# Kernel optimization log

Hardware: AMD Instinct MI355X
Metric: run time of the kernel (lower is better)

The kernel has to match this reference:

```python
import jax, jax.numpy as jnp
import numpy as np

B, K, C, H, W = 16, 32, 256, 80, 80
NH, HD = 8, 32          # num_heads, head_dim (C = NH*HD)
S = 4                   # fixed roi_align sampling grid per 1x1 output bin
EPS = 1e-5


def _bn(x, g, b, m, v):
    # inference-mode BatchNorm2d, NCHW
    s = g / jnp.sqrt(v + EPS)
    return x * s[None, :, None, None] + (b - m * s)[None, :, None, None]


def _bilinear(feat, ys, xs):
    # feat [B,C,H,W]; ys,xs [B,K,S,S] -> [B,K,S,S,C], torchvision roi_align semantics
    Hh, Ww = feat.shape[2], feat.shape[3]
    valid = (ys >= -1.0) & (ys <= Hh) & (xs >= -1.0) & (xs <= Ww)
    y = jnp.clip(ys, 0.0, Hh - 1.0)
    x = jnp.clip(xs, 0.0, Ww - 1.0)
    y0 = jnp.floor(y); x0 = jnp.floor(x)
    y0i = y0.astype(jnp.int32); x0i = x0.astype(jnp.int32)
    y1i = jnp.minimum(y0i + 1, Hh - 1); x1i = jnp.minimum(x0i + 1, Ww - 1)
    ly = y - y0; lx = x - x0; hy = 1.0 - ly; hx = 1.0 - lx
    bidx = jnp.arange(feat.shape[0])[:, None, None, None]
    g = lambda yi, xi: feat[bidx, :, yi, xi]  # -> [B,K,S,S,C]
    val = ((hy * hx)[..., None] * g(y0i, x0i) + (hy * lx)[..., None] * g(y0i, x1i)
           + (ly * hx)[..., None] * g(y1i, x0i) + (ly * lx)[..., None] * g(y1i, x1i))
    return val * valid[..., None].astype(val.dtype)


def _roi_align_1x1(feat, boxes):
    # boxes [B,K,4] normalized xyxy; spatial_scale = 1.0 in the source
    Hh, Ww = feat.shape[2], feat.shape[3]
    sc = jnp.asarray([Ww - 1, Hh - 1, Ww - 1, Hh - 1], feat.dtype)
    ab = boxes * sc
    x1, y1, x2, y2 = ab[..., 0], ab[..., 1], ab[..., 2], ab[..., 3]
    rw = jnp.maximum(x2 - x1, 1.0)
    rh = jnp.maximum(y2 - y1, 1.0)
    grid = (jnp.arange(S, dtype=feat.dtype) + 0.5) / S
    ys = y1[..., None] + grid * rh[..., None]   # [B,K,S]
    xs = x1[..., None] + grid * rw[..., None]
    ys2, xs2 = jnp.broadcast_arrays(ys[..., :, None], xs[..., None, :])  # [B,K,S,S]
    vals = _bilinear(feat, ys2, xs2)            # [B,K,S,S,C]
    return vals.mean(axis=(2, 3)).reshape(feat.shape[0] * boxes.shape[1], -1)


def _gat(nodes, wq, bq, wk, bkp, wv, bv, scale, wo, bo, ln_g, ln_b):
    Bk = nodes.shape[0]
    q = (nodes @ wq.T + bq).reshape(Bk, NH, HD)
    k = (nodes @ wk.T + bkp).reshape(Bk, NH, HD)
    v = (nodes @ wv.T + bv).reshape(Bk, NH, HD)
    scores = jnp.einsum('ihd,jhd->ijh', q, k) * scale
    attn = jax.nn.softmax(scores, axis=1)       # softmax over keys j
    msg = jnp.einsum('ijh,jhd->ihd', attn, v).reshape(Bk, NH * HD)
    y = nodes + msg @ wo.T + bo
    mu = y.mean(-1, keepdims=True)
    var = ((y - mu) ** 2).mean(-1, keepdims=True)
    return (y - mu) / jnp.sqrt(var + EPS) * ln_g + ln_b


def _forward(x, boxes, conv_w, conv_b, bn1_g, bn1_b, bn1_m, bn1_v,
             wq, bq, wk, bkp, wv, bv, scale, wo, bo, ln_g, ln_b,
             rec_w, rec_b, bn2_g, bn2_b, bn2_m, bn2_v):
    feat = jax.lax.conv_general_dilated(
        x, conv_w, (1, 1), 'SAME',
        dimension_numbers=('NCHW', 'OIHW', 'NCHW')) + conv_b[None, :, None, None]
    feat = _bn(feat, bn1_g, bn1_b, bn1_m, bn1_v)
    feat = feat * jax.nn.sigmoid(feat)          # SiLU
    nodes = _roi_align_1x1(feat, boxes)         # [B*K, C]
    enh = _gat(nodes, wq, bq, wk, bkp, wv, bv, scale, wo, bo, ln_g, ln_b)
    f = enh.reshape(B, K, C)
    wts = jax.nn.softmax(f.mean(-1), axis=1)    # [B,K]
    weighted = jnp.einsum('bkc,bk->bc', f, wts)
    # out map is spatially constant -> 1x1 conv + BN collapse to per-sample affine
    y = weighted @ rec_w[:, :, 0, 0].T + rec_b
    s = bn2_g / jnp.sqrt(bn2_v + EPS)
    y = y * s + (bn2_b - bn2_m * s)
    return x + y[:, :, None, None]


def setup_inputs() -> dict:
    key = jax.random.key(0)
    ks = jax.random.split(key, 10)
    x = jax.random.normal(ks[0], (B, C, H, W), jnp.float32)
    bx = jax.random.uniform(ks[1], (B, K, 4), jnp.float32)
    bx = bx.at[:, :, 2:].add(bx[:, :, :2])      # xy2 += xy1
    boxes = jnp.clip(bx, 0.0, 1.0)
    w = lambda k, shp: jax.random.normal(k, shp, jnp.float32) * 0.02
    return {
        'x': x, 'boxes': boxes,
        'conv_w': w(ks[2], (C, C, 3, 3)), 'conv_b': jnp.zeros((C,), jnp.float32),
        'bn1_g': jnp.ones((C,), jnp.float32), 'bn1_b': jnp.zeros((C,), jnp.float32),
        'bn1_m': jnp.zeros((C,), jnp.float32), 'bn1_v': jnp.ones((C,), jnp.float32),
        'wq': w(ks[3], (C, C)), 'bq': jnp.zeros((C,), jnp.float32),
        'wk': w(ks[4], (C, C)), 'bkp': jnp.zeros((C,), jnp.float32),
        'wv': w(ks[5], (C, C)), 'bv': jnp.zeros((C,), jnp.float32),
        'scale': jnp.asarray(1.0 / np.sqrt(HD), jnp.float32),
        'wo': w(ks[6], (C, C)), 'bo': jnp.zeros((C,), jnp.float32),
        'ln_g': jnp.ones((C,), jnp.float32), 'ln_b': jnp.zeros((C,), jnp.float32),
        'rec_w': w(ks[7], (C, C, 1, 1)), 'rec_b': jnp.zeros((C,), jnp.float32),
        'bn2_g': jnp.ones((C,), jnp.float32), 'bn2_b': jnp.zeros((C,), jnp.float32),
        'bn2_m': jnp.zeros((C,), jnp.float32), 'bn2_v': jnp.ones((C,), jnp.float32),
    }


def reference(x, boxes, conv_w, conv_b, bn1_g, bn1_b, bn1_m, bn1_v,
              wq, bq, wk, bkp, wv, bv, scale, wo, bo, ln_g, ln_b,
              rec_w, rec_b, bn2_g, bn2_b, bn2_m, bn2_v):
    return _forward(x, boxes, conv_w, conv_b, bn1_g, bn1_b, bn1_m, bn1_v,
                    wq, bq, wk, bkp, wv, bv, scale, wo, bo, ln_g, ln_b,
                    rec_w, rec_b, bn2_g, bn2_b, bn2_m, bn2_v)
```

## Files before the change

### kernel.cpp

```cpp
#include <hip/hip_runtime.h>

#define EPSV 1e-5f

typedef __attribute__((ext_vector_type(8))) short short8v;
typedef __attribute__((ext_vector_type(4))) float f32x4;

static __device__ __forceinline__ unsigned short f2bf(float f) {
  unsigned int u = __float_as_uint(f);
  u += 0x7fff + ((u >> 16) & 1);
  return (unsigned short)(u >> 16);
}
static __device__ __forceinline__ float bf2f(unsigned short h) {
  return __uint_as_float(((unsigned int)h) << 16);
}

static __device__ __forceinline__ void glds16(const void* g, void* l) {
  __builtin_amdgcn_global_load_lds(
      (const __attribute__((address_space(1))) void*)g,
      (__attribute__((address_space(3))) void*)l, 16, 0, 0);
}

__global__ __launch_bounds__(256) void prep_fused_kernel(
    const float* __restrict__ x, unsigned short* __restrict__ xin,
    const float* __restrict__ cw, unsigned short* __restrict__ Wr,
    float* __restrict__ zpad,
    const float* __restrict__ wq, const float* __restrict__ wk,
    const float* __restrict__ wv, const float* __restrict__ wo,
    const float* __restrict__ rec, float* __restrict__ wT)
{
  __shared__ unsigned short t[80 * 257];
  const int bid = blockIdx.x;
  if (bid < 1280) {
    int b = bid / 80, y = bid - b * 80;
    const float* src = x + (size_t)b * 256 * 6400 + y * 80;
    for (int e = threadIdx.x; e < 256 * 20; e += 256) {
      int c = e / 20;
      int px4 = e - c * 20;
      f32x4 v = *(const f32x4*)&src[(size_t)c * 6400 + px4 * 4];
#pragma unroll
      for (int j = 0; j < 4; ++j)
        t[(px4 * 4 + j) * 257 + c] = f2bf(v[j]);
    }
    __syncthreads();
    unsigned short* dst = xin + (size_t)bid * 80 * 256;
    for (int e = threadIdx.x; e < 80 * 32; e += 256) {
      int px = e >> 5;
      int c8 = e & 31;
      short8v v;
#pragma unroll
      for (int j = 0; j < 8; ++j) v[j] = t[px * 257 + c8 * 8 + j];
      *(short8v*)&dst[px * 256 + c8 * 8] = v;
    }
  } else if (bid < 3584) {
    if (bid == 1280) zpad[threadIdx.x] = 0.f;
    int idx = (bid - 1280) * 256 + threadIdx.x;
    int cil = idx & 31;
    int rest = idx >> 5;
    int co = rest & 255;
    int tcc = rest >> 8;
    int cc = tcc & 7;
    int tt = tcc >> 3;
    int dy = tt / 3, dx = tt - dy * 3;
    int ci = cc * 32 + cil;
    Wr[idx] = f2bf(cw[((co * 256 + ci) * 3 + dy) * 3 + dx]);
  } else {
    int idx = (bid - 3584) * 256 + threadIdx.x;
    int m = idx >> 16;
    int e = idx & 65535;
    int ci = e >> 8, co = e & 255;
    const float* src = (m == 0) ? wq : (m == 1) ? wk : (m == 2) ? wv
                     : (m == 3) ? wo : rec;
    wT[idx] = src[co * 256 + ci];
  }
}

__global__ __launch_bounds__(256, 2) void roiconv_kernel(
    const unsigned short* __restrict__ xin,
    const float* __restrict__ boxes,
    const float* __restrict__ convb,
    const float* __restrict__ bn1g, const float* __restrict__ bn1b,
    const float* __restrict__ bn1m, const float* __restrict__ bn1v,
    const unsigned short* __restrict__ Wr,
    float* __restrict__ nodes)
{
  const int bid = blockIdx.x;
  const int n = (bid & 7) * 64 + (bid >> 3);
  const int b = n >> 5;
  const int tid = threadIdx.x;
  const int w = tid >> 6, lane = tid & 63;
  const int bq = lane >> 4, r16 = lane & 15;

  __shared__ __align__(16) char lds[61696];
  float* wcoef = (float*)(lds + 61440);

  const int px = tid >> 2;
  const float* bx = boxes + n * 4;
  float x1 = bx[0] * 79.f, y1 = bx[1] * 79.f, x2 = bx[2] * 79.f, y2 = bx[3] * 79.f;
  float rwd = fmaxf(x2 - x1, 1.f), rh = fmaxf(y2 - y1, 1.f);
  int s = px >> 2;
  int sy = s >> 2, sx = s & 3;
  float yy = y1 + (sy + 0.5f) * 0.25f * rh;
  float xx = x1 + (sx + 0.5f) * 0.25f * rwd;
  bool valid = (yy >= -1.f) && (yy <= 80.f) && (xx >= -1.f) && (xx <= 80.f);
  float yc = fminf(fmaxf(yy, 0.f), 79.f), xc = fminf(fmaxf(xx, 0.f), 79.f);
  float y0f = floorf(yc), x0f = floorf(xc);
  int y0i = (int)y0f, x0i = (int)x0f;
  int y1i = min(y0i + 1, 79), x1i = min(x0i + 1, 79);
  float ly = yc - y0f, lx = xc - x0f, hy = 1.f - ly, hx = 1.f - lx;
  int py = (px & 2) ? y1i : y0i;
  int pxx = (px & 1) ? x1i : x0i;
  if ((tid & 3) == 0)
    wcoef[px] = ((px & 2) ? ly : hy) * ((px & 1) ? lx : hx) *
                (valid ? 0.0625f : 0.f);

  const int chunk = (tid & 3) ^ ((px >> 1) & 3);
  unsigned ioff[9];
#pragma unroll
  for (int t = 0; t < 9; ++t) {
    int dy = t / 3, dx = t - dy * 3;
    int cy = py + dy - 1, cx = pxx + dx - 1;
    bool ok = ((unsigned)cy < 80u) && ((unsigned)cx < 80u);
    ioff[t] = ok ? (unsigned)((((b * 80 + cy) * 80 + cx) * 256 + chunk * 8) * 2)
                 : 52428800u;
  }
  unsigned woff[4];
#pragma unroll
  for (int i = 0; i < 4; ++i) {
    int s2 = tid + (i << 8);
    int wco = s2 >> 2;
    int wch = (s2 & 3) ^ ((wco >> 1) & 3);
    woff[i] = (unsigned)((wco * 32 + wch * 8) * 2);
  }
  const int laneoff = r16 * 64 + ((bq ^ ((r16 >> 1) & 3)) << 4);
  const char* xinb = (const char*)xin;
  const char* Wrb = (const char*)Wr;
  const int ldst_in = (w << 6) << 4;

  f32x4 acc[4][4];
#pragma unroll
  for (int i = 0; i < 4; ++i)
#pragma unroll
    for (int j = 0; j < 4; ++j)
      acc[i][j] = (f32x4){0.f, 0.f, 0.f, 0.f};

  glds16(xinb + ioff[0], lds + 0 + ldst_in);
#pragma unroll
  for (int i = 0; i < 4; ++i)
    glds16(Wrb + woff[i], lds + 12288 + (((i << 8) + (w << 6)) << 4));
  glds16(xinb + ioff[1], lds + 4096 + ldst_in);
#pragma unroll
  for (int i = 0; i < 4; ++i)
    glds16(Wrb + ((size_t)8 << 14) + woff[i],
           lds + 28672 + (((i << 8) + (w << 6)) << 4));

  for (int cc = 0; cc < 8; ++cc) {
#pragma unroll
    for (int t = 0; t < 9; ++t) {
      const int cb = t % 3;
      const char* inb = lds + cb * 4096;
      const char* wb  = lds + 12288 + cb * 16384;
      if (cc == 7 && t == 8)
        asm volatile("s_waitcnt vmcnt(0)" ::: "memory");
      else
        asm volatile("s_waitcnt vmcnt(5)" ::: "memory");
      __builtin_amdgcn_s_barrier();
      __builtin_amdgcn_sched_barrier(0);
      if (!(cc == 7 && t >= 7)) {
        const int nt = (t + 2 > 8) ? t - 7 : t + 2;
        const int nb = nt % 3;
        const int ncc = cc + (t >= 7 ? 1 : 0);
        char* innx = lds + nb * 4096;
        char* wbn  = lds + 12288 + nb * 16384;
        glds16(xinb + ioff[nt] + ncc * 64, innx + ldst_in);
        const char* wg = Wrb + ((size_t)(nt * 8 + ncc) << 14);
#pragma unroll
        for (int i = 0; i < 4; ++i)
          glds16(wg + woff[i], wbn + (((i << 8) + (w << 6)) << 4));
      }
      const char* pa = inb + laneoff;
      const char* pw = wb + w * 4096 + laneoff;
      short8v af0 = *(const short8v*)(pa);
      short8v af1 = *(const short8v*)(pa + 1024);
      short8v af2 = *(const short8v*)(pa + 2048);
      short8v af3 = *(const short8v*)(pa + 3072);
      short8v wf0 = *(const short8v*)(pw);
      short8v wf1 = *(const short8v*)(pw + 1024);
      short8v wf2 = *(const short8v*)(pw + 2048);
      short8v wf3 = *(const short8v*)(pw + 3072);
      __builtin_amdgcn_s_setprio(1);
      acc[0][0] = __builtin_amdgcn_mfma_f32_16x16x32_bf16(af0, wf0, acc[0][0], 0, 0, 0);
      acc[0][1] = __builtin_amdgcn_mfma_f32_16x16x32_bf16(af0, wf1, acc[0][1], 0, 0, 0);
      acc[0][2] = __builtin_amdgcn_mfma_f32_16x16x32_bf16(af0, wf2, acc[0][2], 0, 0, 0);
      acc[0][3] = __builtin_amdgcn_mfma_f32_16x16x32_bf16(af0, wf3, acc[0][3], 0, 0, 0);
      acc[1][0] = __builtin_amdgcn_mfma_f32_16x16x32_bf16(af1, wf0, acc[1][0], 0, 0, 0);
      acc[1][1] = __builtin_amdgcn_mfma_f32_16x16x32_bf16(af1, wf1, acc[1][1], 0, 0, 0);
      acc[1][2] = __builtin_amdgcn_mfma_f32_16x16x32_bf16(af1, wf2, acc[1][2], 0, 0, 0);
      acc[1][3] = __builtin_amdgcn_mfma_f32_16x16x32_bf16(af1, wf3, acc[1][3], 0, 0, 0);
      acc[2][0] = __builtin_amdgcn_mfma_f32_16x16x32_bf16(af2, wf0, acc[2][0], 0, 0, 0);
      acc[2][1] = __builtin_amdgcn_mfma_f32_16x16x32_bf16(af2, wf1, acc[2][1], 0, 0, 0);
      acc[2][2] = __builtin_amdgcn_mfma_f32_16x16x32_bf16(af2, wf2, acc[2][2], 0, 0, 0);
      acc[2][3] = __builtin_amdgcn_mfma_f32_16x16x32_bf16(af2, wf3, acc[2][3], 0, 0, 0);
      acc[3][0] = __builtin_amdgcn_mfma_f32_16x16x32_bf16(af3, wf0, acc[3][0], 0, 0, 0);
      acc[3][1] = __builtin_amdgcn_mfma_f32_16x16x32_bf16(af3, wf1, acc[3][1], 0, 0, 0);
      acc[3][2] = __builtin_amdgcn_mfma_f32_16x16x32_bf16(af3, wf2, acc[3][2], 0, 0, 0);
      acc[3][3] = __builtin_amdgcn_mfma_f32_16x16x32_bf16(af3, wf3, acc[3][3], 0, 0, 0);
      __builtin_amdgcn_s_setprio(0);
    }
  }
  asm volatile("s_waitcnt vmcnt(0)" ::: "memory");
  __syncthreads();

  unsigned short* ep = (unsigned short*)lds;
#pragma unroll
  for (int cf = 0; cf < 4; ++cf) {
    int co = w * 64 + cf * 16 + r16;
    float sc = bn1g[co] / sqrtf(bn1v[co] + EPSV);
    float sh = bn1b[co] - bn1m[co] * sc;
    float cb = convb[co];
#pragma unroll
    for (int mf = 0; mf < 4; ++mf) {
#pragma unroll
      for (int rg = 0; rg < 4; ++rg) {
        int pxo = mf * 16 + bq * 4 + rg;
        float v = (acc[mf][cf][rg] + cb) * sc + sh;
        v = v / (1.f + __expf(-v));
        ep[pxo * 264 + co] = f2bf(v);
      }
    }
  }
  __syncthreads();
  const int c = tid;
  float val = 0.f;
#pragma unroll
  for (int p = 0; p < 64; ++p)
    val += wcoef[p] * bf2f(ep[p * 264 + c]);
  nodes[n * 256 + c] = val;
}

__global__ __launch_bounds__(256) void qkv_kernel(
    const float* __restrict__ nodes, const float* __restrict__ wT,
    const float* __restrict__ bq, const float* __restrict__ bk,
    const float* __restrict__ bv,
    float* __restrict__ q, float* __restrict__ k, float* __restrict__ v)
{
  const int blk = blockIdx.x;
  const int co = threadIdx.x;
  __shared__ float nd[4][256];
  for (int i = threadIdx.x; i < 1024; i += 256)
    nd[i >> 8][i & 255] = nodes[blk * 1024 + i];
  __syncthreads();
  float aq[4] = {0, 0, 0, 0};
  float ak[4] = {0, 0, 0, 0};
  float av[4] = {0, 0, 0, 0};
  const float* wqT = wT;
  const float* wkT = wT + 65536;
  const float* wvT = wT + 131072;
  for (int ci = 0; ci < 256; ++ci) {
    float wq_ = wqT[ci * 256 + co];
    float wk_ = wkT[ci * 256 + co];
    float wv_ = wvT[ci * 256 + co];
#pragma unroll
    for (int r = 0; r < 4; ++r) {
      float nv = nd[r][ci];
      aq[r] += nv * wq_;
      ak[r] += nv * wk_;
      av[r] += nv * wv_;
    }
  }
  float bq_ = bq[co], bk_ = bk[co], bv_ = bv[co];
#pragma unroll
  for (int r = 0; r < 4; ++r) {
    int n = blk * 4 + r;
    q[n * 256 + co] = aq[r] + bq_;
    k[n * 256 + co] = ak[r] + bk_;
    v[n * 256 + co] = av[r] + bv_;
  }
}

__global__ __launch_bounds__(256) void attn_mh_kernel(
    const float* __restrict__ q, const float* __restrict__ k,
    const float* __restrict__ v, const float* __restrict__ scale_p,
    float* __restrict__ msgs)
{
  const int bid = blockIdx.x;
  const int h = bid & 7, qc = bid >> 3;
  const int q0 = qc * 16;
  const int tid = threadIdx.x;
  __shared__ __align__(16) float Kh[512 * 32];
  __shared__ __align__(16) float Vh[512 * 32];
  __shared__ unsigned short pb[16 * 512];

  for (int idx = tid; idx < 4096; idx += 256) {
    int j = idx >> 3, part = idx & 7;
    int chs = part ^ (j & 7);
    *(f32x4*)&Kh[j * 32 + chs * 4] =
        *(const f32x4*)&k[(size_t)j * 256 + h * 32 + part * 4];
    *(f32x4*)&Vh[j * 32 + chs * 4] =
        *(const f32x4*)&v[(size_t)j * 256 + h * 32 + part * 4];
  }
  const int qi = tid >> 4, l = tid & 15;
  f32x4 qr[8];
#pragma unroll
  for (int p = 0; p < 8; ++p)
    qr[p] = *(const f32x4*)&q[(size_t)(q0 + qi) * 256 + h * 32 + p * 4];
  const float scale = scale_p[0];
  __syncthreads();

  float pj[32];
  float mx = -1e30f;
#pragma unroll
  for (int jj = 0; jj < 32; ++jj) {
    int j = jj * 16 + l;
    const float* kr = &Kh[j * 32];
    int sw = j & 7;
    float s = 0.f;
#pragma unroll
    for (int p = 0; p < 8; ++p) {
      f32x4 kv = *(const f32x4*)&kr[(p ^ sw) * 4];
      s += kv.x * qr[p].x + kv.y * qr[p].y + kv.z * qr[p].z + kv.w * qr[p].w;
    }
    s *= scale;
    pj[jj] = s;
    mx = fmaxf(mx, s);
  }
#pragma unroll
  for (int o = 1; o < 16; o <<= 1) mx = fmaxf(mx, __shfl_xor(mx, o, 16));
  float sum = 0.f;
#pragma unroll
  for (int jj = 0; jj < 32; ++jj) {
    float e = __expf(pj[jj] - mx);
    pj[jj] = e;
    sum += e;
  }
#pragma unroll
  for (int o = 1; o < 16; o <<= 1) sum += __shfl_xor(sum, o, 16);
  float inv = 1.f / sum;
#pragma unroll
  for (int jj = 0; jj < 32; ++jj)
    pb[qi * 512 + jj * 16 + l] = f2bf(pj[jj] * inv);
  __syncthreads();

  float m0 = 0.f, m1 = 0.f;
  const unsigned short* pq = &pb[qi * 512];
  for (int j = 0; j < 512; ++j) {
    float p = bf2f(pq[j]);
    int chs = (l >> 1) ^ (j & 7);
    const float* vr = &Vh[j * 32 + chs * 4 + ((2 * l) & 3)];
    m0 += p * vr[0];
    m1 += p * vr[1];
  }
  float* mo = &msgs[(size_t)(q0 + qi) * 256 + h * 32 + 2 * l];
  mo[0] = m0;
  mo[1] = m1;
}

__global__ __launch_bounds__(256) void outln_kernel(
    const float* __restrict__ msgs, const float* __restrict__ nodes,
    const float* __restrict__ woT, const float* __restrict__ bo,
    const float* __restrict__ lng, const float* __restrict__ lnb,
    float* __restrict__ enh)
{
  const int blk = blockIdx.x;
  const int co = threadIdx.x;
  __shared__ float ms[8][256];
  __shared__ float red1[8][4], red2[8][4];
  for (int i = co; i < 2048; i += 256)
    ms[i >> 8][i & 255] = msgs[blk * 2048 + i];
  __syncthreads();
  float yv[8];
  float bo_ = bo[co];
#pragma unroll
  for (int r = 0; r < 8; ++r)
    yv[r] = nodes[(size_t)(blk * 8 + r) * 256 + co] + bo_;
  for (int ci = 0; ci < 256; ++ci) {
    float w = woT[ci * 256 + co];
#pragma unroll
    for (int r = 0; r < 8; ++r) yv[r] += ms[r][ci] * w;
  }
  const int wv = co >> 6, lane = co & 63;
#pragma unroll
  for (int r = 0; r < 8; ++r) {
    float s1 = yv[r], s2 = yv[r] * yv[r];
#pragma unroll
    for (int o = 1; o < 64; o <<= 1) {
      s1 += __shfl_xor(s1, o);
      s2 += __shfl_xor(s2, o);
    }
    if (lane == 0) { red1[r][wv] = s1; red2[r][wv] = s2; }
  }
  __syncthreads();
  float lg = lng[co], lb = lnb[co];
#pragma unroll
  for (int r = 0; r < 8; ++r) {
    float S1 = red1[r][0] + red1[r][1] + red1[r][2] + red1[r][3];
    float S2 = red2[r][0] + red2[r][1] + red2[r][2] + red2[r][3];
    float mu = S1 * (1.f / 256.f);
    float var = S2 * (1.f / 256.f) - mu * mu;
    enh[(size_t)(blk * 8 + r) * 256 + co] =
        (yv[r] - mu) * rsqrtf(var + EPSV) * lg + lb;
  }
}

__global__ __launch_bounds__(256) void final_kernel(
    const float* __restrict__ enh, const float* __restrict__ recT,
    const float* __restrict__ recb,
    const float* __restrict__ bn2g, const float* __restrict__ bn2b,
    const float* __restrict__ bn2m, const float* __restrict__ bn2v,
    float* __restrict__ yfin)
{
  const int b = blockIdx.x;
  const int tid = threadIdx.x;
  const int wv = tid >> 6, l = tid & 63;
  __shared__ float rm[32], wts[32], wgt[256];
  for (int kk = wv; kk < 32; kk += 4) {
    const float* er = enh + (size_t)(b * 32 + kk) * 256;
    float s = er[l] + er[l + 64] + er[l + 128] + er[l + 192];
#pragma unroll
    for (int o = 1; o < 64; o <<= 1) s += __shfl_xor(s, o);
    if (l == 0) rm[kk] = s * (1.f / 256.f);
  }
  __syncthreads();
  if (tid < 32) {
    float m = rm[tid];
    float mx = m;
#pragma unroll
    for (int o = 1; o < 32; o <<= 1) mx = fmaxf(mx, __shfl_xor(mx, o, 32));
    float e = __expf(m - mx);
    float sm = e;
#pragma unroll
    for (int o = 1; o < 32; o <<= 1) sm += __shfl_xor(sm, o, 32);
    wts[tid] = e / sm;
  }
  __syncthreads();
  float wsum = 0.f;
  for (int kk = 0; kk < 32; ++kk)
    wsum += enh[(size_t)(b * 32 + kk) * 256 + tid] * wts[kk];
  wgt[tid] = wsum;
  __syncthreads();
  const int co = tid;
  float yv = recb[co];
  for (int ci = 0; ci < 256; ++ci)
    yv += wgt[ci] * recT[ci * 256 + co];
  float s = bn2g[co] / sqrtf(bn2v[co] + EPSV);
  yfin[b * 256 + co] = yv * s + (bn2b[co] - bn2m[co] * s);
}

__global__ __launch_bounds__(256) void add_kernel(
    const float* __restrict__ x, const float* __restrict__ yfin,
    float* __restrict__ out)
{
  const int bc = blockIdx.x;
  const float a = yfin[bc];
  const f32x4* xp = (const f32x4*)(x + (size_t)bc * 6400);
  f32x4* op = (f32x4*)(out + (size_t)bc * 6400);
  for (int i = threadIdx.x; i < 1600; i += 256) {
    f32x4 v = xp[i];
    v.x += a; v.y += a; v.z += a; v.w += a;
    op[i] = v;
  }
}

extern "C" void kernel_launch(void* const* d_in, const int* in_sizes, int n_in,
                              void* d_out, int out_size, void* d_ws, size_t ws_size,
                              hipStream_t stream)
{
  const float* x      = (const float*)d_in[0];
  const float* boxes  = (const float*)d_in[1];
  const float* conv_w = (const float*)d_in[2];
  const float* conv_b = (const float*)d_in[3];
  const float* bn1g   = (const float*)d_in[4];
  const float* bn1b   = (const float*)d_in[5];
  const float* bn1m   = (const float*)d_in[6];
  const float* bn1v   = (const float*)d_in[7];
  const float* wq     = (const float*)d_in[8];
  const float* bq     = (const float*)d_in[9];
  const float* wk     = (const float*)d_in[10];
  const float* bkp    = (const float*)d_in[11];
  const float* wv     = (const float*)d_in[12];
  const float* bv     = (const float*)d_in[13];
  const float* scale  = (const float*)d_in[14];
  const float* wo     = (const float*)d_in[15];
  const float* bo     = (const float*)d_in[16];
  const float* lng    = (const float*)d_in[17];
  const float* lnb    = (const float*)d_in[18];
  const float* rec_w  = (const float*)d_in[19];
  const float* rec_b  = (const float*)d_in[20];
  const float* bn2g   = (const float*)d_in[21];
  const float* bn2b   = (const float*)d_in[22];
  const float* bn2m   = (const float*)d_in[23];
  const float* bn2v   = (const float*)d_in[24];
  float* out = (float*)d_out;

  char* ws = (char*)d_ws;
  unsigned short* Wr = (unsigned short*)(ws);
  float* wT    = (float*)(ws + 53608448);
  float* nodes = (float*)(ws + 54919168);
  float* qb    = nodes + 131072;
  float* kb    = qb + 131072;
  float* vb    = kb + 131072;
  float* enh   = vb + 131072;
  float* yfin  = enh + 131072;
  float* msgs  = yfin + 4096;

  unsigned short* xin = (unsigned short*)d_out;
  float* zpad = (float*)((char*)d_out + 52428800);

  hipLaunchKernelGGL(prep_fused_kernel, dim3(4864), dim3(256), 0, stream,
                     x, xin, conv_w, Wr, zpad, wq, wk, wv, wo, rec_w, wT);
  hipLaunchKernelGGL(roiconv_kernel, dim3(512), dim3(256), 0, stream,
                     xin, boxes, conv_b, bn1g, bn1b, bn1m, bn1v, Wr, nodes);
  hipLaunchKernelGGL(qkv_kernel, dim3(128), dim3(256), 0, stream,
                     nodes, wT, bq, bkp, bv, qb, kb, vb);
  hipLaunchKernelGGL(attn_mh_kernel, dim3(256), dim3(256), 0, stream,
                     qb, kb, vb, scale, msgs);
  hipLaunchKernelGGL(outln_kernel, dim3(64), dim3(256), 0, stream,
                     msgs, nodes, wT + 3 * 65536, bo, lng, lnb, enh);
  hipLaunchKernelGGL(final_kernel, dim3(16), dim3(256), 0, stream,
                     enh, wT + 4 * 65536, rec_b, bn2g, bn2b, bn2m, bn2v, yfin);
  hipLaunchKernelGGL(add_kernel, dim3(4096), dim3(256), 0, stream, x, yfin, out);
}
```

Before: 186.7 us.

## Process two ROIs per block so conv weight tiles are shared

Each roiconv block now handles two ROIs with 512 threads arranged as a 2x4 wave grid, so every weight tile staged in LDS serves 128 pixel rows instead of 64. This halves the global weight traffic per ROI and the number of weight loads issued per thread. The cost is a larger LDS footprint, one block per CU, and a grid of 256 blocks, which may leave some CUs idle and lowers occupancy.

New measurement: 182.2 us. 2.4% less time.

```diff
diff --git a/kernel.cpp b/kernel.cpp
--- a/kernel.cpp
+++ b/kernel.cpp
@@ -74,7 +74,7 @@
   }
 }
 
-__global__ __launch_bounds__(256, 2) void roiconv_kernel(
+__global__ __launch_bounds__(512, 1) void roiconv_kernel(
     const unsigned short* __restrict__ xin,
     const float* __restrict__ boxes,
     const float* __restrict__ convb,
@@ -84,20 +84,24 @@
     float* __restrict__ nodes)
 {
   const int bid = blockIdx.x;
-  const int n = (bid & 7) * 64 + (bid >> 3);
+  const int pr = (bid & 7) * 32 + (bid >> 3);
+  const int tid = threadIdx.x;
+  const int nd = tid >> 8;
+  const int n = pr * 2 + nd;
   const int b = n >> 5;
-  const int tid = threadIdx.x;
   const int w = tid >> 6, lane = tid & 63;
   const int bq = lane >> 4, r16 = lane & 15;
-
-  __shared__ __align__(16) char lds[61696];
-  float* wcoef = (float*)(lds + 61440);
-
-  const int px = tid >> 2;
+  const int wr = w >> 2, wc = w & 3;
+
+  __shared__ __align__(16) char lds[74240];
+  float* wcoef = (float*)(lds + 73728);
+  const int INB = 0, WB = 24576;
+
+  const int pc = (tid >> 2) & 63;
   const float* bx = boxes + n * 4;
   float x1 = bx[0] * 79.f, y1 = bx[1] * 79.f, x2 = bx[2] * 79.f, y2 = bx[3] * 79.f;
   float rwd = fmaxf(x2 - x1, 1.f), rh = fmaxf(y2 - y1, 1.f);
-  int s = px >> 2;
+  int s = pc >> 2;
   int sy = s >> 2, sx = s & 3;
   float yy = y1 + (sy + 0.5f) * 0.25f * rh;
   float xx = x1 + (sx + 0.5f) * 0.25f * rwd;
@@ -107,13 +111,13 @@
   int y0i = (int)y0f, x0i = (int)x0f;
   int y1i = min(y0i + 1, 79), x1i = min(x0i + 1, 79);
   float ly = yc - y0f, lx = xc - x0f, hy = 1.f - ly, hx = 1.f - lx;
-  int py = (px & 2) ? y1i : y0i;
-  int pxx = (px & 1) ? x1i : x0i;
+  int py = (pc & 2) ? y1i : y0i;
+  int pxx = (pc & 1) ? x1i : x0i;
   if ((tid & 3) == 0)
-    wcoef[px] = ((px & 2) ? ly : hy) * ((px & 1) ? lx : hx) *
-                (valid ? 0.0625f : 0.f);
-
-  const int chunk = (tid & 3) ^ ((px >> 1) & 3);
+    wcoef[tid >> 2] = ((pc & 2) ? ly : hy) * ((pc & 1) ? lx : hx) *
+                      (valid ? 0.0625f : 0.f);
+
+  const int chunk = (tid & 3) ^ ((pc >> 1) & 3);
   unsigned ioff[9];
 #pragma unroll
   for (int t = 0; t < 9; ++t) {
@@ -123,10 +127,10 @@
     ioff[t] = ok ? (unsigned)((((b * 80 + cy) * 80 + cx) * 256 + chunk * 8) * 2)
                  : 52428800u;
   }
-  unsigned woff[4];
-#pragma unroll
-  for (int i = 0; i < 4; ++i) {
-    int s2 = tid + (i << 8);
+  unsigned woff[2];
+#pragma unroll
+  for (int i = 0; i < 2; ++i) {
+    int s2 = tid + (i << 9);
     int wco = s2 >> 2;
     int wch = (s2 & 3) ^ ((wco >> 1) & 3);
     woff[i] = (unsigned)((wco * 32 + wch * 8) * 2);
@@ -134,7 +138,7 @@
   const int laneoff = r16 * 64 + ((bq ^ ((r16 >> 1) & 3)) << 4);
   const char* xinb = (const char*)xin;
   const char* Wrb = (const char*)Wr;
-  const int ldst_in = (w << 6) << 4;
+  const int ldwave = w << 10;
 
   f32x4 acc[4][4];
 #pragma unroll
@@ -143,42 +147,38 @@
     for (int j = 0; j < 4; ++j)
       acc[i][j] = (f32x4){0.f, 0.f, 0.f, 0.f};
 
-  glds16(xinb + ioff[0], lds + 0 + ldst_in);
-#pragma unroll
-  for (int i = 0; i < 4; ++i)
-    glds16(Wrb + woff[i], lds + 12288 + (((i << 8) + (w << 6)) << 4));
-  glds16(xinb + ioff[1], lds + 4096 + ldst_in);
-#pragma unroll
-  for (int i = 0; i < 4; ++i)
-    glds16(Wrb + ((size_t)8 << 14) + woff[i],
-           lds + 28672 + (((i << 8) + (w << 6)) << 4));
+  glds16(xinb + ioff[0], lds + INB + ldwave);
+  glds16(Wrb + woff[0], lds + WB + ldwave);
+  glds16(Wrb + woff[1], lds + WB + 8192 + ldwave);
+  glds16(xinb + ioff[1], lds + INB + 8192 + ldwave);
+  glds16(Wrb + ((size_t)8 << 14) + woff[0], lds + WB + 16384 + ldwave);
+  glds16(Wrb + ((size_t)8 << 14) + woff[1], lds + WB + 16384 + 8192 + ldwave);
 
   for (int cc = 0; cc < 8; ++cc) {
 #pragma unroll
     for (int t = 0; t < 9; ++t) {
       const int cb = t % 3;
-      const char* inb = lds + cb * 4096;
-      const char* wb  = lds + 12288 + cb * 16384;
+      const char* inb = lds + INB + cb * 8192;
+      const char* wb  = lds + WB + cb * 16384;
       if (cc == 7 && t == 8)
         asm volatile("s_waitcnt vmcnt(0)" ::: "memory");
       else
-        asm volatile("s_waitcnt vmcnt(5)" ::: "memory");
+        asm volatile("s_waitcnt vmcnt(3)" ::: "memory");
       __builtin_amdgcn_s_barrier();
       __builtin_amdgcn_sched_barrier(0);
       if (!(cc == 7 && t >= 7)) {
         const int nt = (t + 2 > 8) ? t - 7 : t + 2;
         const int nb = nt % 3;
         const int ncc = cc + (t >= 7 ? 1 : 0);
-        char* innx = lds + nb * 4096;
-        char* wbn  = lds + 12288 + nb * 16384;
-        glds16(xinb + ioff[nt] + ncc * 64, innx + ldst_in);
+        char* innx = lds + INB + nb * 8192;
+        char* wbn  = lds + WB + nb * 16384;
+        glds16(xinb + ioff[nt] + ncc * 64, innx + ldwave);
         const char* wg = Wrb + ((size_t)(nt * 8 + ncc) << 14);
-#pragma unroll
-        for (int i = 0; i < 4; ++i)
-          glds16(wg + woff[i], wbn + (((i << 8) + (w << 6)) << 4));
+        glds16(wg + woff[0], wbn + ldwave);
+        glds16(wg + woff[1], wbn + 8192 + ldwave);
       }
-      const char* pa = inb + laneoff;
-      const char* pw = wb + w * 4096 + laneoff;
+      const char* pa = inb + wr * 4096 + laneoff;
+      const char* pw = wb + wc * 4096 + laneoff;
       short8v af0 = *(const short8v*)(pa);
       short8v af1 = *(const short8v*)(pa + 1024);
       short8v af2 = *(const short8v*)(pa + 2048);
@@ -207,13 +207,12 @@
       __builtin_amdgcn_s_setprio(0);
     }
   }
-  asm volatile("s_waitcnt vmcnt(0)" ::: "memory");
   __syncthreads();
 
   unsigned short* ep = (unsigned short*)lds;
 #pragma unroll
   for (int cf = 0; cf < 4; ++cf) {
-    int co = w * 64 + cf * 16 + r16;
+    int co = wc * 64 + cf * 16 + r16;
     float sc = bn1g[co] / sqrtf(bn1v[co] + EPSV);
     float sh = bn1b[co] - bn1m[co] * sc;
     float cb = convb[co];
@@ -221,7 +220,7 @@
     for (int mf = 0; mf < 4; ++mf) {
 #pragma unroll
       for (int rg = 0; rg < 4; ++rg) {
-        int pxo = mf * 16 + bq * 4 + rg;
+        int pxo = wr * 64 + mf * 16 + bq * 4 + rg;
         float v = (acc[mf][cf][rg] + cb) * sc + sh;
         v = v / (1.f + __expf(-v));
         ep[pxo * 264 + co] = f2bf(v);
@@ -229,11 +228,11 @@
     }
   }
   __syncthreads();
-  const int c = tid;
+  const int c = tid & 255;
   float val = 0.f;
 #pragma unroll
   for (int p = 0; p < 64; ++p)
-    val += wcoef[p] * bf2f(ep[p * 264 + c]);
+    val += wcoef[nd * 64 + p] * bf2f(ep[(nd * 64 + p) * 264 + c]);
   nodes[n * 256 + c] = val;
 }
 
@@ -507,7 +506,7 @@
 
   hipLaunchKernelGGL(prep_fused_kernel, dim3(4864), dim3(256), 0, stream,
                      x, xin, conv_w, Wr, zpad, wq, wk, wv, wo, rec_w, wT);
-  hipLaunchKernelGGL(roiconv_kernel, dim3(512), dim3(256), 0, stream,
+  hipLaunchKernelGGL(roiconv_kernel, dim3(256), dim3(512), 0, stream,
                      xin, boxes, conv_b, bn1g, bn1b, bn1m, bn1v, Wr, nodes);
   hipLaunchKernelGGL(qkv_kernel, dim3(128), dim3(256), 0, stream,
                      nodes, wT, bq, bkp, bv, qb, kb, vb);
```
